# Optimization experiments

Measured on AMD Instinct MI355X. Metric: run time of the kernel, lower is better.

## Reference

```python
import jax, jax.numpy as jnp
import numpy as np

H = 128      # hidden_channels
C = 5        # input_channels
B = 2048     # batch
G = 10       # grid size


def _conv(x, w, b, pad):
    # x: [B,Cin,H,W], w: [Cout,Cin,kh,kw]
    y = jax.lax.conv_general_dilated(
        x, w, window_strides=(1, 1), padding=[(pad, pad), (pad, pad)],
        dimension_numbers=('NCHW', 'OIHW', 'NCHW'))
    return y + b[None, :, None, None]


def setup_inputs() -> dict:
    key = jax.random.key(0)
    ks = jax.random.split(key, 16)
    s = 0.05  # weight init scale
    inp = {
        'x': jax.random.uniform(ks[0], (B, C, G, G), dtype=jnp.float32),
        'w_p1': jax.random.normal(ks[1], (H, C, 3, 3), jnp.float32) * s,
        'b_p1': jnp.zeros((H,), jnp.float32),
        'w_p2': jax.random.normal(ks[2], (H, H, 3, 3), jnp.float32) * s,
        'b_p2': jnp.zeros((H,), jnp.float32),
        'w_p3': jax.random.normal(ks[3], (H, H, 1, 1), jnp.float32) * s,
        'b_p3': jnp.zeros((H,), jnp.float32),
        'w_u1': jax.random.normal(ks[4], (H, H, 1, 1), jnp.float32) * s,
        'b_u1': jnp.zeros((H,), jnp.float32),
        'w_u2': jax.random.normal(ks[5], (H, H, 1, 1), jnp.float32) * s,
        'b_u2': jnp.zeros((H,), jnp.float32),
        'w_u3': jax.random.normal(ks[6], (H, H, 1, 1), jnp.float32) * s,
        'b_u3': jnp.zeros((H,), jnp.float32),
        'w_u4': jax.random.normal(ks[7], (C, H, 1, 1), jnp.float32) * s,
        'b_u4': jnp.zeros((C,), jnp.float32),
        'steps': 50,
    }
    return inp


def reference(x, w_p1, b_p1, w_p2, b_p2, w_p3, b_p3,
              w_u1, b_u1, w_u2, b_u2, w_u3, b_u3, w_u4, b_u4, steps):
    relu = jax.nn.relu
    steps_f = jnp.float32(steps)

    def step_fn(x, step):
        dx = relu(_conv(x, w_p1, b_p1, 1))
        dx = relu(_conv(dx, w_p2, b_p2, 1))
        dx = relu(_conv(dx, w_p3, b_p3, 0))
        dx = relu(_conv(dx, w_u1, b_u1, 0))
        dx = relu(_conv(dx, w_u2, b_u2, 0))
        dx = relu(_conv(dx, w_u3, b_u3, 0))
        dx = _conv(dx, w_u4, b_u4, 0)
        x = x + dx
        temperature = jnp.maximum(1.0 - step / steps_f, 0.5)
        x = jax.nn.softmax(x / temperature, axis=1)
        return x, x

    x_final, states = jax.lax.scan(step_fn, x, jnp.arange(steps, dtype=jnp.float32))
    # states: [steps, B, C, G, G] — stacked analogue of the python list
    return x_final, states
```

## Files before the change

### kernel.cpp

```cpp
#include <hip/hip_runtime.h>
#include <cstdint>
#include <cstddef>


#define NSAMPLES 2048
#define PM    112
#define ZROW  112
#define HA_OFF 0
#define HB_OFF 28928
#define A1_OFF HB_OFF
#define XS_OFF 57600
#define LDS_TOTAL 62976

typedef __attribute__((ext_vector_type(8))) short bf16x8;
typedef __attribute__((ext_vector_type(4))) float f32x4;
typedef __attribute__((ext_vector_type(2))) unsigned int u32x2;
typedef __attribute__((ext_vector_type(4))) unsigned int u32x4;

#define MFMA16(A, B, C) __builtin_amdgcn_mfma_f32_16x16x32_bf16((A), (B), (C), 0, 0, 0)

__device__ __forceinline__ short f2bf(float f) {
  unsigned u = __float_as_uint(f);
  return (short)((u + 0x7FFFu + ((u >> 16) & 1u)) >> 16);
}

__global__ void prepack_kernel(const float* __restrict__ w, short* __restrict__ dst,
                               int mode, int ntc, int Kact, int Nact, int total) {
  int idx = blockIdx.x * 256 + threadIdx.x;
  if (idx >= total) return;
  int j = idx & 7, l = (idx >> 3) & 63, t = idx >> 9;
  int nt = t % ntc, kt = t / ntc;
  int kg = kt * 32 + (l >> 4) * 8 + j;
  int nn = nt * 16 + (l & 15);
  float v = 0.f;
  if (mode == 0) {
    if (kg < Kact && nn < Nact) v = w[nn * Kact + kg];
  } else if (mode == 1) {
    if (kg < 45) { int s = kg / 5, cin = kg - 5 * s; v = w[nn * 45 + cin * 9 + s]; }
  } else {
    int s = kt >> 2;
    int kk = (kt & 3) * 32 + (l >> 4) * 8 + j;
    v = w[nn * 1152 + kk * 9 + s];
  }
  dst[idx] = f2bf(v);
}

__device__ __forceinline__ void chain_mfma(const bf16x8 (&Wb)[2][4], const f32x4 (&pb)[2],
                                           const char* src, int n, int g16, int swzc,
                                           f32x4 (&acc)[2][7]) {
#pragma unroll
  for (int mt = 0; mt < 2; ++mt)
#pragma unroll
    for (int qt = 0; qt < 7; ++qt) acc[mt][qt] = pb[mt];
#pragma unroll
  for (int kt = 0; kt < 4; ++kt) {
#pragma unroll
    for (int qt = 0; qt < 7; ++qt) {
      bf16x8 Bf = *(const bf16x8*)(src + (16 * qt + n) * 256 + (((kt * 64) | g16) ^ swzc));
      acc[0][qt] = MFMA16(Wb[0][kt], Bf, acc[0][qt]);
      acc[1][qt] = MFMA16(Wb[1][kt], Bf, acc[1][qt]);
    }
  }
}

__device__ __forceinline__ void store_h(const f32x4 (&acc)[2][7], char* dst,
                                        int n, int woff0, int woff1) {
#pragma unroll
  for (int mt = 0; mt < 2; ++mt) {
    int wo = mt ? woff1 : woff0;
#pragma unroll
    for (int qt = 0; qt < 7; ++qt) {
      f32x4 v = acc[mt][qt];
      unsigned lo = (unsigned)(unsigned short)f2bf(fmaxf(v.x, 0.f)) |
                    ((unsigned)(unsigned short)f2bf(fmaxf(v.y, 0.f)) << 16);
      unsigned hi = (unsigned)(unsigned short)f2bf(fmaxf(v.z, 0.f)) |
                    ((unsigned)(unsigned short)f2bf(fmaxf(v.w, 0.f)) << 16);
      u32x2 wv = {lo, hi};
      *(u32x2*)(dst + (16 * qt + n) * 256 + wo) = wv;
    }
  }
}

__global__ __launch_bounds__(256, 2) void nca_kernel(
    const float* __restrict__ x_in,
    const float* __restrict__ b1p, const float* __restrict__ b2p,
    const float* __restrict__ b3p, const float* __restrict__ b4p,
    const float* __restrict__ b5p, const float* __restrict__ b6p,
    const float* __restrict__ b7p,
    const short* __restrict__ W1, const short* __restrict__ W2,
    const short* __restrict__ W3,
    const short* __restrict__ W7,
    const int* __restrict__ steps_ptr, float* __restrict__ d_out) {
  __shared__ __align__(16) char lds[LDS_TOTAL];
  char* hA = lds + HA_OFF;
  char* hB = lds + HB_OFF;
  char* A1 = lds + A1_OFF;
  float* xs = (float*)(lds + XS_OFF);

  const int tid = threadIdx.x;
  const int sample = blockIdx.x;
  const int w = tid >> 6;
  const int l = tid & 63;
  const int n = l & 15;
  const int g = l >> 4;
  const int g16 = g << 4;
  const int swzc = (n & 7) << 4;
  const int steps = *steps_ptr;
  const float steps_f = (float)steps;
  const f32x4 fz = {0.f, 0.f, 0.f, 0.f};

  const int woff0 = ((32 * (2 * w)) | (8 * g)) ^ swzc;
  const int woff1 = ((32 * (2 * w + 1)) | (8 * g)) ^ swzc;

  int rc[7];
#pragma unroll
  for (int qt = 0; qt < 7; ++qt) {
    int p = 16 * qt + n;
    if (p < 100) { int r = p / 10; rc[qt] = r * 32 + (p - 10 * r); }
    else rc[qt] = 0x4000;
  }

  if (tid < 64) *(unsigned*)(hA + ZROW * 256 + tid * 4) = 0;
  for (int i = tid; i < 500; i += 256) {
    int c = i / 100, px = i - 100 * c;
    xs[px * 12 + c] = x_in[(size_t)sample * 500 + i];
  }
  f32x4 b7v = fz;
  if (g == 0) b7v = *(const f32x4*)&b7p[0];
  else if (g == 1) b7v.x = b7p[4];
  __syncthreads();

  for (int step = 0; step < steps; ++step) {
    if (step > 0) {
      size_t sb = 1024000u + ((size_t)(step - 1) * NSAMPLES + sample) * 500u;
      for (int i = tid; i < 500; i += 256) {
        int c = i / 100, px = i - 100 * c;
        __builtin_nontemporal_store(xs[px * 12 + c], &d_out[sb + i]);
      }
    }
    if (tid < PM) {
      int p = tid;
      bool pv = p < 100;
      int pc = pv ? p : 99;
      int r = pc / 10, c0 = pc - 10 * r;
      unsigned short sh[48];
#pragma unroll
      for (int kk = 45; kk < 48; ++kk) sh[kk] = 0;
#pragma unroll
      for (int s = 0; s < 9; ++s) {
        int dr = s / 3 - 1, dc = s - 3 * (s / 3) - 1;
        f32x4 xv = fz; float x4v = 0.f;
        if (pv && (unsigned)(r + dr) < 10u && (unsigned)(c0 + dc) < 10u) {
          const float* xr = &xs[(p + dr * 10 + dc) * 12];
          xv = *(const f32x4*)xr; x4v = xr[4];
        }
        sh[5 * s + 0] = (unsigned short)f2bf(xv.x);
        sh[5 * s + 1] = (unsigned short)f2bf(xv.y);
        sh[5 * s + 2] = (unsigned short)f2bf(xv.z);
        sh[5 * s + 3] = (unsigned short)f2bf(xv.w);
        sh[5 * s + 4] = (unsigned short)f2bf(x4v);
      }
      int swzr = (p & 7) << 4;
      char* arow = A1 + p * 128;
#pragma unroll
      for (int j = 0; j < 6; ++j) {
        u32x4 wv = {(unsigned)sh[8 * j] | ((unsigned)sh[8 * j + 1] << 16),
                    (unsigned)sh[8 * j + 2] | ((unsigned)sh[8 * j + 3] << 16),
                    (unsigned)sh[8 * j + 4] | ((unsigned)sh[8 * j + 5] << 16),
                    (unsigned)sh[8 * j + 6] | ((unsigned)sh[8 * j + 7] << 16)};
        *(u32x4*)(arow + ((16 * j) ^ swzr)) = wv;
      }
      u32x4 z4 = {0, 0, 0, 0};
      *(u32x4*)(arow + (96 ^ swzr)) = z4;
      *(u32x4*)(arow + (112 ^ swzr)) = z4;
    }
    __syncthreads();

    {
      bf16x8 Wf[2][2];
#pragma unroll
      for (int mt = 0; mt < 2; ++mt)
#pragma unroll
        for (int kt = 0; kt < 2; ++kt)
          Wf[mt][kt] = *(const bf16x8*)&W1[((kt * 8 + 2 * w + mt) * 64 + l) * 8];
      f32x4 pb0 = *(const f32x4*)&b1p[16 * (2 * w) + 4 * g];
      f32x4 pb1 = *(const f32x4*)&b1p[16 * (2 * w + 1) + 4 * g];
      f32x4 acc[2][7];
#pragma unroll
      for (int qt = 0; qt < 7; ++qt) { acc[0][qt] = pb0; acc[1][qt] = pb1; }
#pragma unroll
      for (int kt = 0; kt < 2; ++kt) {
#pragma unroll
        for (int qt = 0; qt < 7; ++qt) {
          bf16x8 Bf = *(const bf16x8*)(A1 + (16 * qt + n) * 128 + (((kt * 64) | g16) ^ swzc));
          acc[0][qt] = MFMA16(Wf[0][kt], Bf, acc[0][qt]);
          acc[1][qt] = MFMA16(Wf[1][kt], Bf, acc[1][qt]);
        }
      }
      store_h(acc, hA, n, woff0, woff1);
    }
    __syncthreads();

    {
      f32x4 acc[2][7];
      {
        f32x4 pb0 = *(const f32x4*)&b2p[16 * (2 * w) + 4 * g];
        f32x4 pb1 = *(const f32x4*)&b2p[16 * (2 * w + 1) + 4 * g];
#pragma unroll
        for (int qt = 0; qt < 7; ++qt) { acc[0][qt] = pb0; acc[1][qt] = pb1; }
      }
#pragma unroll 1
      for (int s = 0; s < 9; ++s) {
        int s3 = s / 3;
        int dr = s3 - 1, dc = s - 3 * s3 - 1;
        int doff = dr * 10 + dc;
        const short* Wsl = W2 + s * 16384;
        bf16x8 Wf[2][4];
#pragma unroll
        for (int mt = 0; mt < 2; ++mt)
#pragma unroll
          for (int kt = 0; kt < 4; ++kt)
            Wf[mt][kt] = *(const bf16x8*)&Wsl[((kt * 8 + 2 * w + mt) * 64 + l) * 8];
#pragma unroll
        for (int qt = 0; qt < 7; ++qt) {
          bool ok = ((unsigned)((rc[qt] >> 5) + dr) < 10u) &&
                    ((unsigned)((rc[qt] & 31) + dc) < 10u);
          int prow = ok ? (16 * qt + n + doff) : ZROW;
          const char* rb = hA + prow * 256;
          int swz = (prow & 7) << 4;
#pragma unroll
          for (int kt = 0; kt < 4; ++kt) {
            bf16x8 Bf = *(const bf16x8*)(rb + (((kt * 64) | g16) ^ swz));
            acc[0][qt] = MFMA16(Wf[0][kt], Bf, acc[0][qt]);
            acc[1][qt] = MFMA16(Wf[1][kt], Bf, acc[1][qt]);
          }
        }
      }
      store_h(acc, hB, n, woff0, woff1);
    }
    __syncthreads();

#pragma unroll 1
    for (int li = 0; li < 4; ++li) {
      const short* Wp = W3 + li * 16384;
      const float* bp = (li == 0) ? b3p : (li == 1) ? b4p : (li == 2) ? b5p : b6p;
      const char* src = (li & 1) ? hA : hB;
      char* dst = (li & 1) ? hB : hA;
      bf16x8 Wf[2][4];
#pragma unroll
      for (int mt = 0; mt < 2; ++mt)
#pragma unroll
        for (int kt = 0; kt < 4; ++kt)
          Wf[mt][kt] = *(const bf16x8*)&Wp[((kt * 8 + 2 * w + mt) * 64 + l) * 8];
      f32x4 pb[2];
      pb[0] = *(const f32x4*)&bp[16 * (2 * w) + 4 * g];
      pb[1] = *(const f32x4*)&bp[16 * (2 * w + 1) + 4 * g];
      f32x4 acc[2][7];
      chain_mfma(Wf, pb, src, n, g16, swzc, acc);
      store_h(acc, dst, n, woff0, woff1);
      __syncthreads();
    }

    {
      bf16x8 W7f[4];
#pragma unroll
      for (int kt = 0; kt < 4; ++kt)
        W7f[kt] = *(const bf16x8*)&W7[(kt * 64 + l) * 8];
      float invT = 1.f / fmaxf(1.f - (float)step / steps_f, 0.5f);
#pragma unroll
      for (int rep = 0; rep < 2; ++rep) {
        int qt = 2 * w + rep;
        if (qt < 7) {
          f32x4 a = b7v;
#pragma unroll
          for (int kt = 0; kt < 4; ++kt) {
            bf16x8 Bf = *(const bf16x8*)(hB + (16 * qt + n) * 256 + (((kt * 64) | g16) ^ swzc));
            a = MFMA16(W7f[kt], Bf, a);
          }
          float c4v = __shfl_xor(a.x, 16);
          int px = 16 * qt + n;
          if (g == 0 && px < 100) {
            float* xr = &xs[px * 12];
            f32x4 xo = *(f32x4*)xr; float x4 = xr[4];
            float v0 = (xo.x + a.x) * invT, v1 = (xo.y + a.y) * invT;
            float v2 = (xo.z + a.z) * invT, v3 = (xo.w + a.w) * invT;
            float v4 = (x4 + c4v) * invT;
            float m = fmaxf(fmaxf(fmaxf(v0, v1), fmaxf(v2, v3)), v4);
            float e0 = __expf(v0 - m), e1 = __expf(v1 - m), e2 = __expf(v2 - m);
            float e3 = __expf(v3 - m), e4 = __expf(v4 - m);
            float inv = 1.f / (e0 + e1 + e2 + e3 + e4);
            f32x4 pv = {e0 * inv, e1 * inv, e2 * inv, e3 * inv};
            *(f32x4*)xr = pv; xr[4] = e4 * inv;
          }
        }
      }
    }
    __syncthreads();
  }

  {
    size_t sb = 1024000u + ((size_t)(steps - 1) * NSAMPLES + sample) * 500u;
    size_t fb = (size_t)sample * 500u;
    for (int i = tid; i < 500; i += 256) {
      int c = i / 100, px = i - 100 * c;
      float v = xs[px * 12 + c];
      __builtin_nontemporal_store(v, &d_out[fb + i]);
      __builtin_nontemporal_store(v, &d_out[sb + i]);
    }
  }
}

extern "C" void kernel_launch(void* const* d_in, const int* in_sizes, int n_in,
                              void* d_out, int out_size, void* d_ws, size_t ws_size,
                              hipStream_t stream) {
  const float* x   = (const float*)d_in[0];
  const float* wp1 = (const float*)d_in[1];
  const float* bp1 = (const float*)d_in[2];
  const float* wp2 = (const float*)d_in[3];
  const float* bp2 = (const float*)d_in[4];
  const float* wp3 = (const float*)d_in[5];
  const float* bp3 = (const float*)d_in[6];
  const float* wu1 = (const float*)d_in[7];
  const float* bu1 = (const float*)d_in[8];
  const float* wu2 = (const float*)d_in[9];
  const float* bu2 = (const float*)d_in[10];
  const float* wu3 = (const float*)d_in[11];
  const float* bu3 = (const float*)d_in[12];
  const float* wu4 = (const float*)d_in[13];
  const float* bu4 = (const float*)d_in[14];
  const int* steps = (const int*)d_in[15];

  short* W1 = (short*)d_ws;
  short* W2 = W1 + 8192;
  short* W3 = W2 + 147456;
  short* W4 = W3 + 16384;
  short* W5 = W4 + 16384;
  short* W6 = W5 + 16384;
  short* W7 = W6 + 16384;

  prepack_kernel<<<(8192   + 255) / 256, 256, 0, stream>>>(wp1, W1, 1, 8, 45,   128, 8192);
  prepack_kernel<<<(147456 + 255) / 256, 256, 0, stream>>>(wp2, W2, 2, 8, 1152, 128, 147456);
  prepack_kernel<<<(16384  + 255) / 256, 256, 0, stream>>>(wp3, W3, 0, 8, 128,  128, 16384);
  prepack_kernel<<<(16384  + 255) / 256, 256, 0, stream>>>(wu1, W4, 0, 8, 128,  128, 16384);
  prepack_kernel<<<(16384  + 255) / 256, 256, 0, stream>>>(wu2, W5, 0, 8, 128,  128, 16384);
  prepack_kernel<<<(16384  + 255) / 256, 256, 0, stream>>>(wu3, W6, 0, 8, 128,  128, 16384);
  prepack_kernel<<<(2048   + 255) / 256, 256, 0, stream>>>(wu4, W7, 0, 1, 128,  5,   2048);

  nca_kernel<<<NSAMPLES, 256, 0, stream>>>(
      x, bp1, bp2, bp3, bu1, bu2, bu3, bu4,
      W1, W2, W3, W7, steps, (float*)d_out);
}
```

Baseline: 5.240 ms.

## Double-buffer weight register loads across layers and simplify LDS addressing

Weight fragments for the next conv slice or layer now load into alternating register sets (Wa/Wb) while the current slice's MFMAs run. This hides global/L2 latency for weights that were previously loaded right before use. The change also precomputes swizzled LDS addresses, uses v_cvt_pk_bf16_f32 for packing, and unrolls the 3x3 conv slice loop and the 1x1 layer chain. These raise register pressure, and the waves_per_eu attribute replaces the min-blocks launch bound, which may affect occupancy or cause spills.

```diff
diff --git a/kernel.cpp b/kernel.cpp
--- a/kernel.cpp
+++ b/kernel.cpp
@@ -4,8 +4,7 @@
 
 
 #define NSAMPLES 2048
-#define PM    112
-#define ZROW  112
+#define ZROW_BASE 28672
 #define HA_OFF 0
 #define HB_OFF 28928
 #define A1_OFF HB_OFF
@@ -17,7 +16,16 @@
 typedef __attribute__((ext_vector_type(2))) unsigned int u32x2;
 typedef __attribute__((ext_vector_type(4))) unsigned int u32x4;
 
-#define MFMA16(A, B, C) __builtin_amdgcn_mfma_f32_16x16x32_bf16((A), (B), (C), 0, 0, 0)
+#define MFMA16(A,B,C) __builtin_amdgcn_mfma_f32_16x16x32_bf16((A),(B),(C),0,0,0)
+
+__device__ __forceinline__ unsigned pk2(float a, float b) {
+  unsigned r;
+  asm("v_cvt_pk_bf16_f32 %0, %1, %2" : "=v"(r) : "v"(a), "v"(b));
+  return r;
+}
+__device__ __forceinline__ unsigned pk2r(float a, float b) {
+  return pk2(fmaxf(a, 0.f), fmaxf(b, 0.f));
+}
 
 __device__ __forceinline__ short f2bf(float f) {
   unsigned u = __float_as_uint(f);
@@ -45,43 +53,80 @@
   dst[idx] = f2bf(v);
 }
 
-__device__ __forceinline__ void chain_mfma(const bf16x8 (&Wb)[2][4], const f32x4 (&pb)[2],
-                                           const char* src, int n, int g16, int swzc,
-                                           f32x4 (&acc)[2][7]) {
+__device__ __forceinline__ void load_w4(bf16x8 (&W)[2][4], const short* __restrict__ p,
+                                        int w, int l) {
 #pragma unroll
   for (int mt = 0; mt < 2; ++mt)
 #pragma unroll
-    for (int qt = 0; qt < 7; ++qt) acc[mt][qt] = pb[mt];
+    for (int kt = 0; kt < 4; ++kt)
+      W[mt][kt] = *(const bf16x8*)&p[((kt * 8 + 2 * w + mt) * 64 + l) * 8];
+}
+__device__ __forceinline__ void load_w2(bf16x8 (&W)[2][2], const short* __restrict__ p,
+                                        int w, int l) {
+#pragma unroll
+  for (int mt = 0; mt < 2; ++mt)
+#pragma unroll
+    for (int kt = 0; kt < 2; ++kt)
+      W[mt][kt] = *(const bf16x8*)&p[((kt * 8 + 2 * w + mt) * 64 + l) * 8];
+}
+__device__ __forceinline__ void load_b(f32x4 (&pb)[2], const float* __restrict__ bp,
+                                       int w, int g) {
+  pb[0] = *(const f32x4*)&bp[16 * (2 * w) + 4 * g];
+  pb[1] = *(const f32x4*)&bp[16 * (2 * w + 1) + 4 * g];
+}
+
+__device__ __forceinline__ void chain_mfma(const bf16x8 (&W)[2][4], const f32x4 (&pb)[2],
+                                           const char* lds, int rdb, f32x4 (&acc)[2][7]) {
+#pragma unroll
+  for (int qt = 0; qt < 7; ++qt) { acc[0][qt] = pb[0]; acc[1][qt] = pb[1]; }
 #pragma unroll
   for (int kt = 0; kt < 4; ++kt) {
+    const char* src = lds + (rdb ^ (kt << 6));
 #pragma unroll
     for (int qt = 0; qt < 7; ++qt) {
-      bf16x8 Bf = *(const bf16x8*)(src + (16 * qt + n) * 256 + (((kt * 64) | g16) ^ swzc));
-      acc[0][qt] = MFMA16(Wb[0][kt], Bf, acc[0][qt]);
-      acc[1][qt] = MFMA16(Wb[1][kt], Bf, acc[1][qt]);
-    }
-  }
-}
-
-__device__ __forceinline__ void store_h(const f32x4 (&acc)[2][7], char* dst,
-                                        int n, int woff0, int woff1) {
+      bf16x8 Bf = *(const bf16x8*)(src + qt * 4096);
+      acc[0][qt] = MFMA16(W[0][kt], Bf, acc[0][qt]);
+      acc[1][qt] = MFMA16(W[1][kt], Bf, acc[1][qt]);
+    }
+  }
+}
+
+__device__ __forceinline__ void store_h(const f32x4 (&acc)[2][7], char* lds,
+                                        int wb0, int wb1) {
 #pragma unroll
   for (int mt = 0; mt < 2; ++mt) {
-    int wo = mt ? woff1 : woff0;
+    char* d = lds + (mt ? wb1 : wb0);
 #pragma unroll
     for (int qt = 0; qt < 7; ++qt) {
       f32x4 v = acc[mt][qt];
-      unsigned lo = (unsigned)(unsigned short)f2bf(fmaxf(v.x, 0.f)) |
-                    ((unsigned)(unsigned short)f2bf(fmaxf(v.y, 0.f)) << 16);
-      unsigned hi = (unsigned)(unsigned short)f2bf(fmaxf(v.z, 0.f)) |
-                    ((unsigned)(unsigned short)f2bf(fmaxf(v.w, 0.f)) << 16);
-      u32x2 wv = {lo, hi};
-      *(u32x2*)(dst + (16 * qt + n) * 256 + wo) = wv;
-    }
-  }
-}
-
-__global__ __launch_bounds__(256, 2) void nca_kernel(
+      u32x2 wv = {pk2r(v.x, v.y), pk2r(v.z, v.w)};
+      *(u32x2*)(d + qt * 4096) = wv;
+    }
+  }
+}
+
+__device__ __forceinline__ void c2_slice(const bf16x8 (&W)[2][4], f32x4 (&acc)[2][7],
+                                         const char* lds, const int (&rc)[7],
+                                         const int (&zadj)[7], int n, int g16, int s) {
+  const int dr = s / 3 - 1, dc = s % 3 - 1;
+  const int ps = n + dr * 10 + dc;
+  const int bs = HA_OFF + ps * 256 + (g16 ^ ((ps & 7) << 4));
+#pragma unroll
+  for (int qt = 0; qt < 7; ++qt) {
+    bool ok = ((unsigned)((rc[qt] >> 5) + dr) < 10u) &&
+              ((unsigned)((rc[qt] & 31) + dc) < 10u);
+    int va = ok ? bs : zadj[qt];
+#pragma unroll
+    for (int kt = 0; kt < 4; ++kt) {
+      bf16x8 Bf = *(const bf16x8*)(lds + (va ^ (kt << 6)) + qt * 4096);
+      acc[0][qt] = MFMA16(W[0][kt], Bf, acc[0][qt]);
+      acc[1][qt] = MFMA16(W[1][kt], Bf, acc[1][qt]);
+    }
+  }
+}
+
+__global__ __launch_bounds__(256) __attribute__((amdgpu_waves_per_eu(2)))
+void nca_kernel(
     const float* __restrict__ x_in,
     const float* __restrict__ b1p, const float* __restrict__ b2p,
     const float* __restrict__ b3p, const float* __restrict__ b4p,
@@ -92,9 +137,6 @@
     const short* __restrict__ W7,
     const int* __restrict__ steps_ptr, float* __restrict__ d_out) {
   __shared__ __align__(16) char lds[LDS_TOTAL];
-  char* hA = lds + HA_OFF;
-  char* hB = lds + HB_OFF;
-  char* A1 = lds + A1_OFF;
   float* xs = (float*)(lds + XS_OFF);
 
   const int tid = threadIdx.x;
@@ -109,8 +151,16 @@
   const float steps_f = (float)steps;
   const f32x4 fz = {0.f, 0.f, 0.f, 0.f};
 
-  const int woff0 = ((32 * (2 * w)) | (8 * g)) ^ swzc;
-  const int woff1 = ((32 * (2 * w + 1)) | (8 * g)) ^ swzc;
+  const int rdA = HA_OFF + n * 256 + (g16 ^ swzc);
+  const int rdB = HB_OFF + n * 256 + (g16 ^ swzc);
+  const int rd1 = A1_OFF + n * 128 + (g16 ^ swzc);
+  const int wcol0 = ((64 * w) | (8 * g)) ^ swzc;
+  const int wcol1 = ((64 * w + 32) | (8 * g)) ^ swzc;
+  const int wbA0 = HA_OFF + n * 256 + wcol0, wbA1 = HA_OFF + n * 256 + wcol1;
+  const int wbB0 = HB_OFF + n * 256 + wcol0, wbB1 = HB_OFF + n * 256 + wcol1;
+  int zadj[7];
+#pragma unroll
+  for (int qt = 0; qt < 7; ++qt) zadj[qt] = HA_OFF + ZROW_BASE + g16 - 4096 * qt;
 
   int rc[7];
 #pragma unroll
@@ -119,55 +169,57 @@
     if (p < 100) { int r = p / 10; rc[qt] = r * 32 + (p - 10 * r); }
     else rc[qt] = 0x4000;
   }
-
-  if (tid < 64) *(unsigned*)(hA + ZROW * 256 + tid * 4) = 0;
-  for (int i = tid; i < 500; i += 256) {
-    int c = i / 100, px = i - 100 * c;
-    xs[px * 12 + c] = x_in[(size_t)sample * 500 + i];
-  }
+  const int cA = tid / 100, pA = tid - 100 * cA;
+  const int cB = (tid + 256) / 100, pB = tid + 256 - 100 * cB;
+  const int offA = pA * 12 + cA, offB = pB * 12 + cB;
+
+  if (tid < 64) *(unsigned*)(lds + HA_OFF + ZROW_BASE + tid * 4) = 0;
+  xs[offA] = x_in[(size_t)sample * 500 + tid];
+  if (tid < 244) xs[offB] = x_in[(size_t)sample * 500 + tid + 256];
   f32x4 b7v = fz;
   if (g == 0) b7v = *(const f32x4*)&b7p[0];
   else if (g == 1) b7v.x = b7p[4];
   __syncthreads();
 
+  bf16x8 Wa[2][4], Wb[2][4], Wc1[2][2], W7f[4];
+  f32x4 pbc1[2], pbc2[2], pbN[2];
+
   for (int step = 0; step < steps; ++step) {
+    load_w2(Wc1, W1, w, l);
+    load_b(pbc1, b1p, w, g);
+    load_w4(Wa, W2, w, l);
+    load_b(pbc2, b2p, w, g);
     if (step > 0) {
       size_t sb = 1024000u + ((size_t)(step - 1) * NSAMPLES + sample) * 500u;
-      for (int i = tid; i < 500; i += 256) {
-        int c = i / 100, px = i - 100 * c;
-        __builtin_nontemporal_store(xs[px * 12 + c], &d_out[sb + i]);
-      }
-    }
-    if (tid < PM) {
-      int p = tid;
-      bool pv = p < 100;
-      int pc = pv ? p : 99;
-      int r = pc / 10, c0 = pc - 10 * r;
-      unsigned short sh[48];
-#pragma unroll
-      for (int kk = 45; kk < 48; ++kk) sh[kk] = 0;
+      __builtin_nontemporal_store(xs[offA], &d_out[sb + tid]);
+      if (tid < 244) __builtin_nontemporal_store(xs[offB], &d_out[sb + tid + 256]);
+    }
+    if (tid < 112) {
+      const int p = tid;
+      const bool pv = p < 100;
+      const int pc = pv ? p : 99;
+      const int r = pc / 10, c0 = pc - 10 * r;
+      float val[48];
 #pragma unroll
       for (int s = 0; s < 9; ++s) {
-        int dr = s / 3 - 1, dc = s - 3 * (s / 3) - 1;
+        const int dr = s / 3 - 1, dc = s % 3 - 1;
         f32x4 xv = fz; float x4v = 0.f;
         if (pv && (unsigned)(r + dr) < 10u && (unsigned)(c0 + dc) < 10u) {
           const float* xr = &xs[(p + dr * 10 + dc) * 12];
           xv = *(const f32x4*)xr; x4v = xr[4];
         }
-        sh[5 * s + 0] = (unsigned short)f2bf(xv.x);
-        sh[5 * s + 1] = (unsigned short)f2bf(xv.y);
-        sh[5 * s + 2] = (unsigned short)f2bf(xv.z);
-        sh[5 * s + 3] = (unsigned short)f2bf(xv.w);
-        sh[5 * s + 4] = (unsigned short)f2bf(x4v);
+        val[5*s+0] = xv.x; val[5*s+1] = xv.y; val[5*s+2] = xv.z;
+        val[5*s+3] = xv.w; val[5*s+4] = x4v;
       }
-      int swzr = (p & 7) << 4;
-      char* arow = A1 + p * 128;
+      val[45] = val[46] = val[47] = 0.f;
+      unsigned wd[24];
+#pragma unroll
+      for (int i = 0; i < 24; ++i) wd[i] = pk2(val[2*i], val[2*i+1]);
+      const int swzr = (p & 7) << 4;
+      char* arow = lds + A1_OFF + p * 128;
 #pragma unroll
       for (int j = 0; j < 6; ++j) {
-        u32x4 wv = {(unsigned)sh[8 * j] | ((unsigned)sh[8 * j + 1] << 16),
-                    (unsigned)sh[8 * j + 2] | ((unsigned)sh[8 * j + 3] << 16),
-                    (unsigned)sh[8 * j + 4] | ((unsigned)sh[8 * j + 5] << 16),
-                    (unsigned)sh[8 * j + 6] | ((unsigned)sh[8 * j + 7] << 16)};
+        u32x4 wv = {wd[4*j], wd[4*j+1], wd[4*j+2], wd[4*j+3]};
         *(u32x4*)(arow + ((16 * j) ^ swzr)) = wv;
       }
       u32x4 z4 = {0, 0, 0, 0};
@@ -177,104 +229,84 @@
     __syncthreads();
 
     {
-      bf16x8 Wf[2][2];
-#pragma unroll
-      for (int mt = 0; mt < 2; ++mt)
-#pragma unroll
-        for (int kt = 0; kt < 2; ++kt)
-          Wf[mt][kt] = *(const bf16x8*)&W1[((kt * 8 + 2 * w + mt) * 64 + l) * 8];
-      f32x4 pb0 = *(const f32x4*)&b1p[16 * (2 * w) + 4 * g];
-      f32x4 pb1 = *(const f32x4*)&b1p[16 * (2 * w + 1) + 4 * g];
-      f32x4 acc[2][7];
-#pragma unroll
-      for (int qt = 0; qt < 7; ++qt) { acc[0][qt] = pb0; acc[1][qt] = pb1; }
+      load_w4(Wb, W2 + 16384, w, l);
+      f32x4 acc[2][7];
+#pragma unroll
+      for (int qt = 0; qt < 7; ++qt) { acc[0][qt] = pbc1[0]; acc[1][qt] = pbc1[1]; }
 #pragma unroll
       for (int kt = 0; kt < 2; ++kt) {
+        const char* src = lds + (rd1 ^ (kt << 6));
 #pragma unroll
         for (int qt = 0; qt < 7; ++qt) {
-          bf16x8 Bf = *(const bf16x8*)(A1 + (16 * qt + n) * 128 + (((kt * 64) | g16) ^ swzc));
-          acc[0][qt] = MFMA16(Wf[0][kt], Bf, acc[0][qt]);
-          acc[1][qt] = MFMA16(Wf[1][kt], Bf, acc[1][qt]);
+          bf16x8 Bf = *(const bf16x8*)(src + qt * 2048);
+          acc[0][qt] = MFMA16(Wc1[0][kt], Bf, acc[0][qt]);
+          acc[1][qt] = MFMA16(Wc1[1][kt], Bf, acc[1][qt]);
         }
       }
-      store_h(acc, hA, n, woff0, woff1);
-    }
-    __syncthreads();
-
-    {
-      f32x4 acc[2][7];
-      {
-        f32x4 pb0 = *(const f32x4*)&b2p[16 * (2 * w) + 4 * g];
-        f32x4 pb1 = *(const f32x4*)&b2p[16 * (2 * w + 1) + 4 * g];
-#pragma unroll
-        for (int qt = 0; qt < 7; ++qt) { acc[0][qt] = pb0; acc[1][qt] = pb1; }
-      }
-#pragma unroll 1
-      for (int s = 0; s < 9; ++s) {
-        int s3 = s / 3;
-        int dr = s3 - 1, dc = s - 3 * s3 - 1;
-        int doff = dr * 10 + dc;
-        const short* Wsl = W2 + s * 16384;
-        bf16x8 Wf[2][4];
-#pragma unroll
-        for (int mt = 0; mt < 2; ++mt)
-#pragma unroll
-          for (int kt = 0; kt < 4; ++kt)
-            Wf[mt][kt] = *(const bf16x8*)&Wsl[((kt * 8 + 2 * w + mt) * 64 + l) * 8];
-#pragma unroll
-        for (int qt = 0; qt < 7; ++qt) {
-          bool ok = ((unsigned)((rc[qt] >> 5) + dr) < 10u) &&
-                    ((unsigned)((rc[qt] & 31) + dc) < 10u);
-          int prow = ok ? (16 * qt + n + doff) : ZROW;
-          const char* rb = hA + prow * 256;
-          int swz = (prow & 7) << 4;
-#pragma unroll
-          for (int kt = 0; kt < 4; ++kt) {
-            bf16x8 Bf = *(const bf16x8*)(rb + (((kt * 64) | g16) ^ swz));
-            acc[0][qt] = MFMA16(Wf[0][kt], Bf, acc[0][qt]);
-            acc[1][qt] = MFMA16(Wf[1][kt], Bf, acc[1][qt]);
-          }
-        }
-      }
-      store_h(acc, hB, n, woff0, woff1);
-    }
-    __syncthreads();
-
-#pragma unroll 1
-    for (int li = 0; li < 4; ++li) {
-      const short* Wp = W3 + li * 16384;
-      const float* bp = (li == 0) ? b3p : (li == 1) ? b4p : (li == 2) ? b5p : b6p;
-      const char* src = (li & 1) ? hA : hB;
-      char* dst = (li & 1) ? hB : hA;
-      bf16x8 Wf[2][4];
-#pragma unroll
-      for (int mt = 0; mt < 2; ++mt)
-#pragma unroll
-        for (int kt = 0; kt < 4; ++kt)
-          Wf[mt][kt] = *(const bf16x8*)&Wp[((kt * 8 + 2 * w + mt) * 64 + l) * 8];
-      f32x4 pb[2];
-      pb[0] = *(const f32x4*)&bp[16 * (2 * w) + 4 * g];
-      pb[1] = *(const f32x4*)&bp[16 * (2 * w + 1) + 4 * g];
-      f32x4 acc[2][7];
-      chain_mfma(Wf, pb, src, n, g16, swzc, acc);
-      store_h(acc, dst, n, woff0, woff1);
-      __syncthreads();
-    }
-
-    {
-      bf16x8 W7f[4];
+      store_h(acc, lds, wbA0, wbA1);
+    }
+    __syncthreads();
+
+    {
+      f32x4 acc[2][7];
+#pragma unroll
+      for (int qt = 0; qt < 7; ++qt) { acc[0][qt] = pbc2[0]; acc[1][qt] = pbc2[1]; }
+      c2_slice(Wa, acc, lds, rc, zadj, n, g16, 0); load_w4(Wa, W2 + 2 * 16384, w, l);
+      c2_slice(Wb, acc, lds, rc, zadj, n, g16, 1); load_w4(Wb, W2 + 3 * 16384, w, l);
+      c2_slice(Wa, acc, lds, rc, zadj, n, g16, 2); load_w4(Wa, W2 + 4 * 16384, w, l);
+      c2_slice(Wb, acc, lds, rc, zadj, n, g16, 3); load_w4(Wb, W2 + 5 * 16384, w, l);
+      c2_slice(Wa, acc, lds, rc, zadj, n, g16, 4); load_w4(Wa, W2 + 6 * 16384, w, l);
+      c2_slice(Wb, acc, lds, rc, zadj, n, g16, 5); load_w4(Wb, W2 + 7 * 16384, w, l);
+      c2_slice(Wa, acc, lds, rc, zadj, n, g16, 6); load_w4(Wa, W2 + 8 * 16384, w, l);
+      c2_slice(Wb, acc, lds, rc, zadj, n, g16, 7);
+      load_w4(Wb, W3, w, l); load_b(pbN, b3p, w, g);
+      c2_slice(Wa, acc, lds, rc, zadj, n, g16, 8);
+      store_h(acc, lds, wbB0, wbB1);
+    }
+    __syncthreads();
+
+    {
+      load_w4(Wa, W3 + 16384, w, l); load_b(pbc2, b4p, w, g);
+      f32x4 acc[2][7];
+      chain_mfma(Wb, pbN, lds, rdB, acc);
+      store_h(acc, lds, wbA0, wbA1);
+    }
+    __syncthreads();
+    {
+      load_w4(Wb, W3 + 2 * 16384, w, l); load_b(pbN, b5p, w, g);
+      f32x4 acc[2][7];
+      chain_mfma(Wa, pbc2, lds, rdA, acc);
+      store_h(acc, lds, wbB0, wbB1);
+    }
+    __syncthreads();
+    {
+      load_w4(Wa, W3 + 3 * 16384, w, l); load_b(pbc2, b6p, w, g);
+      f32x4 acc[2][7];
+      chain_mfma(Wb, pbN, lds, rdB, acc);
+      store_h(acc, lds, wbA0, wbA1);
+    }
+    __syncthreads();
+    {
 #pragma unroll
       for (int kt = 0; kt < 4; ++kt)
         W7f[kt] = *(const bf16x8*)&W7[(kt * 64 + l) * 8];
+      f32x4 acc[2][7];
+      chain_mfma(Wa, pbc2, lds, rdA, acc);
+      store_h(acc, lds, wbB0, wbB1);
+    }
+    __syncthreads();
+
+    {
       float invT = 1.f / fmaxf(1.f - (float)step / steps_f, 0.5f);
 #pragma unroll
       for (int rep = 0; rep < 2; ++rep) {
         int qt = 2 * w + rep;
         if (qt < 7) {
           f32x4 a = b7v;
+          int va7 = rdB + qt * 4096;
 #pragma unroll
           for (int kt = 0; kt < 4; ++kt) {
-            bf16x8 Bf = *(const bf16x8*)(hB + (16 * qt + n) * 256 + (((kt * 64) | g16) ^ swzc));
+            bf16x8 Bf = *(const bf16x8*)(lds + (va7 ^ (kt << 6)));
             a = MFMA16(W7f[kt], Bf, a);
           }
           float c4v = __shfl_xor(a.x, 16);
@@ -301,11 +333,13 @@
   {
     size_t sb = 1024000u + ((size_t)(steps - 1) * NSAMPLES + sample) * 500u;
     size_t fb = (size_t)sample * 500u;
-    for (int i = tid; i < 500; i += 256) {
-      int c = i / 100, px = i - 100 * c;
-      float v = xs[px * 12 + c];
-      __builtin_nontemporal_store(v, &d_out[fb + i]);
-      __builtin_nontemporal_store(v, &d_out[sb + i]);
+    float vA = xs[offA];
+    __builtin_nontemporal_store(vA, &d_out[fb + tid]);
+    __builtin_nontemporal_store(vA, &d_out[sb + tid]);
+    if (tid < 244) {
+      float vB = xs[offB];
+      __builtin_nontemporal_store(vB, &d_out[fb + tid + 256]);
+      __builtin_nontemporal_store(vB, &d_out[sb + tid + 256]);
     }
   }
 }
```

After: 9.516 ms. 81.6% more time.
